# Kernel optimization log

Hardware: AMD Instinct MI355X
Metric: run time of the kernel (lower is better)

Reference implementation:

```python
import jax, jax.numpy as jnp
import numpy as np

T, B, OBS, H, FC = 128, 512, 1024, 512, 512
LN_EPS = 1e-6  # flax LayerNorm default


def setup_inputs() -> dict:
    key = jax.random.key(0)
    ks = jax.random.split(key, 8)
    sc = lambda k, shape, s: jax.random.normal(k, shape, jnp.float32) * s
    return dict(
        hidden=jnp.zeros((B, H), jnp.float32),  # GRUCell.initialize_carry -> zeros
        world_state=jax.random.normal(ks[0], (T, B, OBS), jnp.float32),
        dones=jax.random.bernoulli(ks[1], 0.05, (T, B)),
        Wd=sc(ks[2], (OBS, H), 1.0 / np.sqrt(OBS)),
        bd=jnp.zeros((H,), jnp.float32),
        ln_scale=jnp.ones((H,), jnp.float32),
        ln_bias=jnp.zeros((H,), jnp.float32),
        Wi=sc(ks[3], (H, 3 * H), 1.0 / np.sqrt(H)),  # input-side GRU weights [r|z|n]
        bi=jnp.zeros((3 * H,), jnp.float32),
        Wh=sc(ks[4], (H, 3 * H), 1.0 / np.sqrt(H)),  # hidden-side GRU weights [r|z|n]
        bhn=jnp.zeros((H,), jnp.float32),            # flax GRU: only hn dense has bias
        Wc1=sc(ks[5], (H, FC), 1.0 / np.sqrt(H)),
        bc1=jnp.zeros((FC,), jnp.float32),
        Wc2=sc(ks[6], (FC, 1), 1.0 / np.sqrt(FC)),
        bc2=jnp.zeros((1,), jnp.float32),
    )


def reference(hidden, world_state, dones, Wd, bd, ln_scale, ln_bias,
              Wi, bi, Wh, bhn, Wc1, bc1, Wc2, bc2):
    # Embed: Dense -> relu -> LayerNorm, applied to all timesteps at once
    emb = jax.nn.relu(world_state @ Wd + bd)                      # [T,B,H]
    mu = emb.mean(-1, keepdims=True)
    var = ((emb - mu) ** 2).mean(-1, keepdims=True)
    emb = (emb - mu) * jax.lax.rsqrt(var + LN_EPS) * ln_scale + ln_bias

    # Precompute input-side GRU projections for all steps (hoisted out of scan)
    xproj = emb @ Wi + bi                                         # [T,B,3H]

    def step(h, inputs):
        xp, done = inputs
        h = jnp.where(done[:, None], 0.0, h)                      # reset carry on done
        xr, xz, xn = jnp.split(xp, 3, axis=-1)
        hr, hz, hn = jnp.split(h @ Wh, 3, axis=-1)                # [B,H] each
        r = jax.nn.sigmoid(xr + hr)
        z = jax.nn.sigmoid(xz + hz)
        n = jnp.tanh(xn + r * (hn + bhn))
        h_new = (1.0 - z) * n + z * h
        return h_new, h_new

    h_last, ys = jax.lax.scan(step, hidden, (xproj, dones))       # ys: [T,B,H]

    critic = jax.nn.relu(ys @ Wc1 + bc1)                          # [T,B,FC]
    value = jnp.squeeze(critic @ Wc2 + bc2, axis=-1)              # [T,B]
    return h_last, value
```

## Files before the change

### kernel.cpp

```cpp
#include <hip/hip_runtime.h>
#include <stdint.h>

#define T_STEPS 128
#define BATCH   512
#define OBSD    1024
#define HD      512
#define FCD     512
#define MROWS   (T_STEPS * BATCH)

typedef unsigned short ushort_t;
typedef __attribute__((ext_vector_type(8))) short bf16x8;
typedef __attribute__((ext_vector_type(4))) float f32x4;
typedef __attribute__((ext_vector_type(2))) uint32_t u32x2;

__device__ inline ushort_t f2bf(float f) {
    union { float f; uint32_t u; } v; v.f = f;
    uint32_t r = v.u + 0x7FFFu + ((v.u >> 16) & 1u);
    return (ushort_t)(r >> 16);
}
__device__ inline float bf2f(ushort_t h) {
    union { uint32_t u; float f; } v; v.u = ((uint32_t)h) << 16;
    return v.f;
}
__device__ inline float fsigmoid(float x) {
    x = fminf(fmaxf(x, -30.f), 30.f);
    return 1.f / (1.f + __expf(-x));
}
__device__ inline float ftanh(float x) {
    float e = __expf(fminf(fmaxf(2.f * x, -30.f), 30.f));
    return (e - 1.f) / (e + 1.f);
}
__device__ inline uint32_t cvt_pk_bf16(float lo, float hi) {
    uint32_t r;
    asm("v_cvt_pk_bf16_f32 %0, %1, %2" : "=v"(r) : "v"(lo), "v"(hi));
    return r;
}
__device__ inline void gload16(const void* g, void* l) {
    __builtin_amdgcn_global_load_lds(
        (const __attribute__((address_space(1))) uint32_t*)g,
        (__attribute__((address_space(3))) uint32_t*)l, 16, 0, 0);
}

__global__ void transpose_to_bf16(const float* __restrict__ in,
                                  ushort_t* __restrict__ out, int R, int C) {
    __shared__ float tile[32][33];
    int tx = threadIdx.x, ty = threadIdx.y;
    int c0 = blockIdx.x * 32, r0 = blockIdx.y * 32;
    for (int yy = 0; yy < 4; ++yy)
        tile[ty + 8 * yy][tx] = in[(size_t)(r0 + ty + 8 * yy) * C + c0 + tx];
    __syncthreads();
    for (int yy = 0; yy < 4; ++yy)
        out[(size_t)(c0 + ty + 8 * yy) * R + r0 + tx] = f2bf(tile[tx][ty + 8 * yy]);
}

__global__ void init_misc(float* __restrict__ v, const float* __restrict__ bc2,
                          unsigned* __restrict__ bar) {
    int i = blockIdx.x * blockDim.x + threadIdx.x;
    if (i < MROWS) v[i] = bc2[0];
    if (i < 2048) bar[i] = 0u;
}

template <int K, int EPI, bool AF32>
__global__ __launch_bounds__(256, 2) void gemm128(
    const void* __restrict__ Aptr, const ushort_t* __restrict__ BT,
    const float* __restrict__ bias, ushort_t* __restrict__ Cout, int ldc,
    const float* __restrict__ wc2, float* __restrict__ value) {
    __shared__ __align__(16) ushort_t Als[128][32];
    __shared__ __align__(16) ushort_t Bls[128][32];
    int tid = threadIdx.x;
    int wave = tid >> 6, lane = tid & 63, quad = lane >> 4, l16 = lane & 15;
    int wr = wave >> 1, wc = wave & 1;
    int bm = blockIdx.y * 128, bn = blockIdx.x * 128;

    f32x4 acc[4][4];
#pragma unroll
    for (int m = 0; m < 4; ++m)
#pragma unroll
        for (int n = 0; n < 4; ++n) acc[m][n] = (f32x4){0.f, 0.f, 0.f, 0.f};

    int srow = tid >> 2;
    int sk = (tid & 3) * 8;
    const ushort_t* Bt0 = &BT[(size_t)(bn + srow) * K + sk];
    const ushort_t* Bt1 = &BT[(size_t)(bn + 64 + srow) * K + sk];
    char* AlsDst = (char*)&Als[0][0] + tid * 16;
    char* BlsDst = (char*)&Bls[0][0] + tid * 16;
    const ushort_t* At0 = nullptr;
    const ushort_t* At1 = nullptr;
    if constexpr (!AF32) {
        const ushort_t* A = (const ushort_t*)Aptr;
        At0 = &A[(size_t)(bm + srow) * K + sk];
        At1 = &A[(size_t)(bm + 64 + srow) * K + sk];
    }

#pragma unroll 1
    for (int k0 = 0; k0 < K; k0 += 32) {
        if constexpr (AF32) {
            const float* A = (const float*)Aptr;
#pragma unroll
            for (int j = 0; j < 4; ++j) {
                int f = tid + 256 * j;
                int r = f >> 3, c4 = f & 7;
                float4 av =
                    *(const float4*)&A[(size_t)(bm + r) * K + k0 + c4 * 4];
                u32x2 w;
                w[0] = cvt_pk_bf16(av.x, av.y);
                w[1] = cvt_pk_bf16(av.z, av.w);
                *(u32x2*)&Als[r][c4 * 4] = w;
            }
        } else {
            gload16(At0 + k0, AlsDst);
            gload16(At1 + k0, AlsDst + 4096);
        }
        gload16(Bt0 + k0, BlsDst);
        gload16(Bt1 + k0, BlsDst + 4096);
        __syncthreads();

        bf16x8 af[4], bfr[4];
#pragma unroll
        for (int m = 0; m < 4; ++m)
            af[m] = *(const bf16x8*)&Als[wr * 64 + m * 16 + l16][quad * 8];
#pragma unroll
        for (int n = 0; n < 4; ++n)
            bfr[n] = *(const bf16x8*)&Bls[wc * 64 + n * 16 + l16][quad * 8];
#pragma unroll
        for (int m = 0; m < 4; ++m)
#pragma unroll
            for (int n = 0; n < 4; ++n)
                acc[m][n] = __builtin_amdgcn_mfma_f32_16x16x32_bf16(
                    af[m], bfr[n], acc[m][n], 0, 0, 0);
        __syncthreads();
    }

    int rbase = bm + wr * 64 + quad * 4;
    if constexpr (EPI == 0 || EPI == 1) {
#pragma unroll
        for (int n = 0; n < 4; ++n) {
            int col = bn + wc * 64 + n * 16 + l16;
            float bv = bias[col];
#pragma unroll
            for (int m = 0; m < 4; ++m) {
#pragma unroll
                for (int i = 0; i < 4; ++i) {
                    float v = acc[m][n][i] + bv;
                    if constexpr (EPI == 0) v = fmaxf(v, 0.f);
                    Cout[(size_t)(rbase + m * 16 + i) * ldc + col] = f2bf(v);
                }
            }
        }
    } else {
        float s[4][4];
#pragma unroll
        for (int m = 0; m < 4; ++m)
#pragma unroll
            for (int i = 0; i < 4; ++i) s[m][i] = 0.f;
#pragma unroll
        for (int n = 0; n < 4; ++n) {
            int col = bn + wc * 64 + n * 16 + l16;
            float bv = bias[col], w2 = wc2[col];
#pragma unroll
            for (int m = 0; m < 4; ++m)
#pragma unroll
                for (int i = 0; i < 4; ++i)
                    s[m][i] += fmaxf(acc[m][n][i] + bv, 0.f) * w2;
        }
#pragma unroll
        for (int m = 0; m < 4; ++m)
#pragma unroll
            for (int i = 0; i < 4; ++i) {
                float v = s[m][i];
                v += __shfl_xor(v, 1);
                v += __shfl_xor(v, 2);
                v += __shfl_xor(v, 4);
                v += __shfl_xor(v, 8);
                if (l16 == 0) atomicAdd(&value[rbase + m * 16 + i], v);
            }
    }
}

__global__ __launch_bounds__(256) void ln_kernel(ushort_t* __restrict__ emb,
                                                 const float* __restrict__ scale,
                                                 const float* __restrict__ biasv) {
    int wave = threadIdx.x >> 6, lane = threadIdx.x & 63;
    size_t row = (size_t)blockIdx.x * 4 + wave;
    ushort_t* p = &emb[row * HD + lane * 8];
    bf16x8 xv = *(const bf16x8*)p;
    float x[8];
    float sum = 0.f, sq = 0.f;
    for (int j = 0; j < 8; ++j) {
        x[j] = bf2f((ushort_t)xv[j]);
        sum += x[j];
        sq += x[j] * x[j];
    }
    for (int off = 32; off > 0; off >>= 1) {
        sum += __shfl_xor(sum, off);
        sq += __shfl_xor(sq, off);
    }
    float mean = sum * (1.f / 512.f);
    float var = fmaxf(sq * (1.f / 512.f) - mean * mean, 0.f);
    float inv = rsqrtf(var + 1e-6f);
    bf16x8 ov;
    for (int j = 0; j < 8; ++j) {
        int col = lane * 8 + j;
        ov[j] = (short)f2bf((x[j] - mean) * inv * scale[col] + biasv[col]);
    }
    *(bf16x8*)p = ov;
}

__global__ __launch_bounds__(256, 1) void scan_coop(
    const float* __restrict__ hidden, const int* __restrict__ dones,
    const ushort_t* __restrict__ WhT, const float* __restrict__ bhn,
    const ushort_t* __restrict__ xproj, ushort_t* __restrict__ ys,
    float* __restrict__ hlast, ushort_t* hb0, ushort_t* hb1,
    unsigned* bar) {
    int tid = threadIdx.x;
    int wave = tid >> 6, lane = tid & 63, quad = lane >> 4, l16 = lane & 15;
    int bid = blockIdx.x;
    int bg = bid & 7, cg = bid >> 3;
    int row0 = bg * 64 + wave * 16;
    int col0 = cg * 16;

    bf16x8 wR[16], wZ[16], wN[16];
    {
        const ushort_t* w0 = &WhT[(size_t)(col0 + l16) * 512 + quad * 8];
#pragma unroll
        for (int kt = 0; kt < 16; ++kt) {
            wR[kt] = *(const bf16x8*)&w0[kt * 32];
            wZ[kt] = *(const bf16x8*)&w0[262144 + kt * 32];
            wN[kt] = *(const bf16x8*)&w0[524288 + kt * 32];
        }
    }

    float mast[4];
    int rbase = row0 + quad * 4;
#pragma unroll
    for (int i = 0; i < 4; ++i) {
        float h0 = hidden[(size_t)(rbase + i) * HD + col0 + l16];
        mast[i] = dones[rbase + i] ? 0.f : h0;
    }
    float bhnv = bhn[col0 + l16];

    unsigned* flg = &bar[(unsigned)((bg * 4 + wave) * 32)];

#pragma unroll
    for (int i = 0; i < 4; ++i) {
        unsigned u = f2bf(mast[i]);
        unsigned p1 = __shfl_xor((int)u, 1);
        unsigned u32 = u | (p1 << 16);
        unsigned hi = __shfl_xor((int)u32, 2);
        if ((l16 & 3) == 0) {
            unsigned long long q =
                (unsigned long long)u32 | ((unsigned long long)hi << 32);
            __hip_atomic_store(
                (unsigned long long*)&hb0[(size_t)(rbase + i) * HD + col0 + l16],
                q, __ATOMIC_RELAXED, __HIP_MEMORY_SCOPE_AGENT);
        }
    }
    asm volatile("s_waitcnt vmcnt(0)" ::: "memory");
    if (lane == 0)
        __hip_atomic_store(&flg[cg], 1u, __ATOMIC_RELAXED,
                           __HIP_MEMORY_SCOPE_AGENT);
    float xr[4], xz[4], xn[4];
    int dn_nxt[4];
#pragma unroll
    for (int i = 0; i < 4; ++i) {
        size_t m = (size_t)(rbase + i);
        const ushort_t* xp = &xproj[m * 1536 + col0 + l16];
        xr[i] = bf2f(xp[0]);
        xz[i] = bf2f(xp[512]);
        xn[i] = bf2f(xp[1024]);
        dn_nxt[i] = dones[BATCH + rbase + i];
    }
    asm volatile("" ::: "memory");

    for (int t = 0; t < T_STEPS; ++t) {
        {
            unsigned tgt = (unsigned)(t + 1);
            for (;;) {
                unsigned f = __hip_atomic_load(&flg[lane & 31], __ATOMIC_RELAXED,
                                               __HIP_MEMORY_SCOPE_AGENT);
                if (__ballot(f >= tgt) == ~0ull) break;
                __builtin_amdgcn_s_sleep(1);
            }
        }
        asm volatile("" ::: "memory");
        ushort_t* rbuf = (t & 1) ? hb1 : hb0;
        ushort_t* wnext = (t & 1) ? hb0 : hb1;

        bf16x8 afr[16];
        {
            const ushort_t* ap =
                &rbuf[(size_t)(row0 + l16) * HD + quad * 8];
            asm volatile(
                "global_load_dwordx4 %0, %16, off sc0 sc1\n\t"
                "global_load_dwordx4 %1, %16, off offset:64 sc0 sc1\n\t"
                "global_load_dwordx4 %2, %16, off offset:128 sc0 sc1\n\t"
                "global_load_dwordx4 %3, %16, off offset:192 sc0 sc1\n\t"
                "global_load_dwordx4 %4, %16, off offset:256 sc0 sc1\n\t"
                "global_load_dwordx4 %5, %16, off offset:320 sc0 sc1\n\t"
                "global_load_dwordx4 %6, %16, off offset:384 sc0 sc1\n\t"
                "global_load_dwordx4 %7, %16, off offset:448 sc0 sc1\n\t"
                "global_load_dwordx4 %8, %16, off offset:512 sc0 sc1\n\t"
                "global_load_dwordx4 %9, %16, off offset:576 sc0 sc1\n\t"
                "global_load_dwordx4 %10, %16, off offset:640 sc0 sc1\n\t"
                "global_load_dwordx4 %11, %16, off offset:704 sc0 sc1\n\t"
                "global_load_dwordx4 %12, %16, off offset:768 sc0 sc1\n\t"
                "global_load_dwordx4 %13, %16, off offset:832 sc0 sc1\n\t"
                "global_load_dwordx4 %14, %16, off offset:896 sc0 sc1\n\t"
                "global_load_dwordx4 %15, %16, off offset:960 sc0 sc1\n\t"
                "s_waitcnt vmcnt(0)"
                : "=&v"(afr[0]), "=&v"(afr[1]), "=&v"(afr[2]), "=&v"(afr[3]),
                  "=&v"(afr[4]), "=&v"(afr[5]), "=&v"(afr[6]), "=&v"(afr[7]),
                  "=&v"(afr[8]), "=&v"(afr[9]), "=&v"(afr[10]), "=&v"(afr[11]),
                  "=&v"(afr[12]), "=&v"(afr[13]), "=&v"(afr[14]), "=&v"(afr[15])
                : "v"(ap)
                : "memory");
        }
        f32x4 aR = (f32x4){0.f, 0.f, 0.f, 0.f};
        f32x4 aZ = (f32x4){0.f, 0.f, 0.f, 0.f};
        f32x4 aN = (f32x4){0.f, 0.f, 0.f, 0.f};
#pragma unroll
        for (int kt = 0; kt < 16; ++kt) {
            aR = __builtin_amdgcn_mfma_f32_16x16x32_bf16(afr[kt], wR[kt], aR, 0, 0, 0);
            aZ = __builtin_amdgcn_mfma_f32_16x16x32_bf16(afr[kt], wZ[kt], aZ, 0, 0, 0);
            aN = __builtin_amdgcn_mfma_f32_16x16x32_bf16(afr[kt], wN[kt], aN, 0, 0, 0);
        }

        unsigned long long qpk[4];
        float hnew[4];
#pragma unroll
        for (int i = 0; i < 4; ++i) {
            float r = fsigmoid(xr[i] + aR[i]);
            float z = fsigmoid(xz[i] + aZ[i]);
            float n = ftanh(xn[i] + r * (aN[i] + bhnv));
            hnew[i] = (1.f - z) * n + z * mast[i];
            unsigned u = f2bf(hnew[i]);
            unsigned p1 = __shfl_xor((int)u, 1);
            unsigned u32 = u | (p1 << 16);
            unsigned hi = __shfl_xor((int)u32, 2);
            qpk[i] = (unsigned long long)u32 | ((unsigned long long)hi << 32);
            mast[i] = (t < T_STEPS - 1 && dn_nxt[i]) ? 0.f : hnew[i];
        }
        if (t < T_STEPS - 1 && (l16 & 3) == 0) {
#pragma unroll
            for (int i = 0; i < 4; ++i) {
                unsigned long long qp = dn_nxt[i] ? 0ull : qpk[i];
                __hip_atomic_store(
                    (unsigned long long*)&wnext[(size_t)(rbase + i) * HD +
                                                col0 + l16],
                    qp, __ATOMIC_RELAXED, __HIP_MEMORY_SCOPE_AGENT);
            }
        }
        asm volatile("s_waitcnt vmcnt(0)" ::: "memory");
        if (t < T_STEPS - 1 && lane == 0)
            __hip_atomic_store(&flg[cg], (unsigned)(t + 2), __ATOMIC_RELAXED,
                               __HIP_MEMORY_SCOPE_AGENT);
        asm volatile("" ::: "memory");
        if ((l16 & 3) == 0) {
#pragma unroll
            for (int i = 0; i < 4; ++i) {
                size_t m = (size_t)t * BATCH + rbase + i;
                *(unsigned long long*)&ys[m * HD + col0 + l16] = qpk[i];
            }
        }
        if (t < T_STEPS - 1) {
            int tn = t + 1;
            int td = (t + 2 < T_STEPS) ? t + 2 : T_STEPS - 1;
#pragma unroll
            for (int i = 0; i < 4; ++i) {
                size_t m = (size_t)tn * BATCH + rbase + i;
                const ushort_t* xp = &xproj[m * 1536 + col0 + l16];
                xr[i] = bf2f(xp[0]);
                xz[i] = bf2f(xp[512]);
                xn[i] = bf2f(xp[1024]);
                dn_nxt[i] = dones[td * BATCH + rbase + i];
            }
        }
        asm volatile("" ::: "memory");
    }
#pragma unroll
    for (int i = 0; i < 4; ++i)
        hlast[(size_t)(rbase + i) * HD + col0 + l16] = mast[i];
}

extern "C" void kernel_launch(void* const* d_in, const int* in_sizes, int n_in,
                              void* d_out, int out_size, void* d_ws,
                              size_t ws_size, hipStream_t stream) {
    const float* hidden      = (const float*)d_in[0];
    const float* world_state = (const float*)d_in[1];
    const int*   dones       = (const int*)d_in[2];
    const float* Wd  = (const float*)d_in[3];
    const float* bd  = (const float*)d_in[4];
    const float* lns = (const float*)d_in[5];
    const float* lnb = (const float*)d_in[6];
    const float* Wi  = (const float*)d_in[7];
    const float* bi  = (const float*)d_in[8];
    const float* Wh  = (const float*)d_in[9];
    const float* bhn = (const float*)d_in[10];
    const float* Wc1 = (const float*)d_in[11];
    const float* bc1 = (const float*)d_in[12];
    const float* Wc2 = (const float*)d_in[13];
    const float* bc2 = (const float*)d_in[14];

    float* out_h = (float*)d_out;
    float* out_v = out_h + BATCH * HD;

    char* ws = (char*)d_ws;
    ushort_t* WdT   = (ushort_t*)(ws + 0);
    ushort_t* WiT   = (ushort_t*)(ws + 1048576);
    ushort_t* WhT   = (ushort_t*)(ws + 2621440);
    ushort_t* Wc1T  = (ushort_t*)(ws + 4194304);
    unsigned* bar   = (unsigned*)(ws + 4718592);
    ushort_t* hb0   = (ushort_t*)(ws + 4726784);
    ushort_t* hb1   = (ushort_t*)(ws + 5251072);
    ushort_t* xproj = (ushort_t*)(ws + 8388608);
    ushort_t* emb   = (ushort_t*)(ws + 209715200);
    ushort_t* ysb   = emb;

    dim3 tb(32, 8);
    transpose_to_bf16<<<dim3(16, 32), tb, 0, stream>>>(Wd, WdT, OBSD, HD);
    transpose_to_bf16<<<dim3(48, 16), tb, 0, stream>>>(Wi, WiT, HD, 1536);
    transpose_to_bf16<<<dim3(48, 16), tb, 0, stream>>>(Wh, WhT, HD, 1536);
    transpose_to_bf16<<<dim3(16, 16), tb, 0, stream>>>(Wc1, Wc1T, HD, FCD);
    init_misc<<<256, 256, 0, stream>>>(out_v, bc2, bar);

    gemm128<OBSD, 0, true><<<dim3(HD / 128, MROWS / 128), 256, 0, stream>>>(
        world_state, WdT, bd, emb, HD, nullptr, nullptr);
    ln_kernel<<<MROWS / 4, 256, 0, stream>>>(emb, lns, lnb);
    gemm128<HD, 1, false><<<dim3(1536 / 128, MROWS / 128), 256, 0, stream>>>(
        emb, WiT, bi, xproj, 1536, nullptr, nullptr);
    scan_coop<<<dim3(256), dim3(256), 0, stream>>>(
        hidden, dones, WhT, bhn, xproj, ysb, out_h, hb0, hb1, bar);
    gemm128<HD, 2, false><<<dim3(FCD / 128, MROWS / 128), 256, 0, stream>>>(
        ysb, Wc1T, bc1, nullptr, 0, Wc2, out_v);
}
```

Baseline: 1.415 ms.

## Stage recurrent weights in LDS and prefetch next-step xproj before MFMAs

Stops holding the per-block slices of the recurrent weight matrix in registers (48 bf16x8 vectors per lane) and stages them once into shared memory, read back each step inside the MFMA loop. This frees a large block of VGPRs. The loads of next-step xproj and dones move from after the h publish to right after the hidden-state load, so their latency overlaps the MFMA chain. The spin-wait sleep is also lengthened. The cost is extra LDS reads on the serial critical path every step, and longer sleeps may add wakeup latency to the barrier.

```diff
diff --git a/kernel.cpp b/kernel.cpp
--- a/kernel.cpp
+++ b/kernel.cpp
@@ -212,6 +212,7 @@
     const ushort_t* __restrict__ xproj, ushort_t* __restrict__ ys,
     float* __restrict__ hlast, ushort_t* hb0, ushort_t* hb1,
     unsigned* bar) {
+    __shared__ __align__(16) ushort_t Wls[48][520];
     int tid = threadIdx.x;
     int wave = tid >> 6, lane = tid & 63, quad = lane >> 4, l16 = lane & 15;
     int bid = blockIdx.x;
@@ -219,15 +220,11 @@
     int row0 = bg * 64 + wave * 16;
     int col0 = cg * 16;
 
-    bf16x8 wR[16], wZ[16], wN[16];
-    {
-        const ushort_t* w0 = &WhT[(size_t)(col0 + l16) * 512 + quad * 8];
-#pragma unroll
-        for (int kt = 0; kt < 16; ++kt) {
-            wR[kt] = *(const bf16x8*)&w0[kt * 32];
-            wZ[kt] = *(const bf16x8*)&w0[262144 + kt * 32];
-            wN[kt] = *(const bf16x8*)&w0[524288 + kt * 32];
-        }
+    for (int idx = tid; idx < 48 * 64; idx += 256) {
+        int c = idx >> 6, ck = (idx & 63) * 8;
+        int g = c >> 4, lc = c & 15;
+        *(bf16x8*)&Wls[c][ck] =
+            *(const bf16x8*)&WhT[(size_t)(g * 512 + col0 + lc) * 512 + ck];
     }
 
     float mast[4];
@@ -270,7 +267,7 @@
         xn[i] = bf2f(xp[1024]);
         dn_nxt[i] = dones[BATCH + rbase + i];
     }
-    asm volatile("" ::: "memory");
+    __syncthreads();
 
     for (int t = 0; t < T_STEPS; ++t) {
         {
@@ -279,7 +276,7 @@
                 unsigned f = __hip_atomic_load(&flg[lane & 31], __ATOMIC_RELAXED,
                                                __HIP_MEMORY_SCOPE_AGENT);
                 if (__ballot(f >= tgt) == ~0ull) break;
-                __builtin_amdgcn_s_sleep(1);
+                __builtin_amdgcn_s_sleep(2);
             }
         }
         asm volatile("" ::: "memory");
@@ -315,14 +312,34 @@
                 : "v"(ap)
                 : "memory");
         }
+
+        float xr2[4], xz2[4], xn2[4];
+        int dn2[4];
+        if (t < T_STEPS - 1) {
+            int tn = t + 1;
+            int td = (t + 2 < T_STEPS) ? t + 2 : T_STEPS - 1;
+#pragma unroll
+            for (int i = 0; i < 4; ++i) {
+                size_t m = (size_t)tn * BATCH + rbase + i;
+                const ushort_t* xp = &xproj[m * 1536 + col0 + l16];
+                xr2[i] = bf2f(xp[0]);
+                xz2[i] = bf2f(xp[512]);
+                xn2[i] = bf2f(xp[1024]);
+                dn2[i] = dones[td * BATCH + rbase + i];
+            }
+        }
+
         f32x4 aR = (f32x4){0.f, 0.f, 0.f, 0.f};
         f32x4 aZ = (f32x4){0.f, 0.f, 0.f, 0.f};
         f32x4 aN = (f32x4){0.f, 0.f, 0.f, 0.f};
 #pragma unroll
         for (int kt = 0; kt < 16; ++kt) {
-            aR = __builtin_amdgcn_mfma_f32_16x16x32_bf16(afr[kt], wR[kt], aR, 0, 0, 0);
-            aZ = __builtin_amdgcn_mfma_f32_16x16x32_bf16(afr[kt], wZ[kt], aZ, 0, 0, 0);
-            aN = __builtin_amdgcn_mfma_f32_16x16x32_bf16(afr[kt], wN[kt], aN, 0, 0, 0);
+            bf16x8 bR = *(const bf16x8*)&Wls[l16][kt * 32 + quad * 8];
+            bf16x8 bZ = *(const bf16x8*)&Wls[16 + l16][kt * 32 + quad * 8];
+            bf16x8 bN = *(const bf16x8*)&Wls[32 + l16][kt * 32 + quad * 8];
+            aR = __builtin_amdgcn_mfma_f32_16x16x32_bf16(afr[kt], bR, aR, 0, 0, 0);
+            aZ = __builtin_amdgcn_mfma_f32_16x16x32_bf16(afr[kt], bZ, aZ, 0, 0, 0);
+            aN = __builtin_amdgcn_mfma_f32_16x16x32_bf16(afr[kt], bN, aN, 0, 0, 0);
         }
 
         unsigned long long qpk[4];
@@ -363,16 +380,10 @@
             }
         }
         if (t < T_STEPS - 1) {
-            int tn = t + 1;
-            int td = (t + 2 < T_STEPS) ? t + 2 : T_STEPS - 1;
 #pragma unroll
             for (int i = 0; i < 4; ++i) {
-                size_t m = (size_t)tn * BATCH + rbase + i;
-                const ushort_t* xp = &xproj[m * 1536 + col0 + l16];
-                xr[i] = bf2f(xp[0]);
-                xz[i] = bf2f(xp[512]);
-                xn[i] = bf2f(xp[1024]);
-                dn_nxt[i] = dones[td * BATCH + rbase + i];
+                xr[i] = xr2[i]; xz[i] = xz2[i]; xn[i] = xn2[i];
+                dn_nxt[i] = dn2[i];
             }
         }
         asm volatile("" ::: "memory");
```

After: 1.601 ms. 1.13x slower.
